# Performance work log

Hardware: AMD Instinct MI355X
Metric: run time of the kernel (lower is better)

The kernel has to match this reference:

```python
import jax, jax.numpy as jnp
import numpy as np

B, S, D_IN, HEAD_DIM = 4, 4096, 1024, 128

def setup_inputs() -> dict:
    key = jax.random.key(0)
    k1, k2, k3, k4 = jax.random.split(key, 4)
    x = jax.random.normal(k1, (B, S, D_IN), dtype=jnp.float32)
    # nn.Parameter(torch.rand(...)) -> uniform [0,1)
    W_query = jax.random.uniform(k2, (D_IN, HEAD_DIM), dtype=jnp.float32)
    W_key = jax.random.uniform(k3, (D_IN, HEAD_DIM), dtype=jnp.float32)
    W_value = jax.random.uniform(k4, (D_IN, HEAD_DIM), dtype=jnp.float32)
    return {"x": x, "W_query": W_query, "W_key": W_key, "W_value": W_value}

def reference(x, W_query, W_key, W_value):
    # x: [B,S,d_in]; W_*: [d_in,head_dim]
    queries = jnp.einsum('bsd,dh->bsh', x, W_query)
    keys = jnp.einsum('bsd,dh->bsh', x, W_key)
    values = jnp.einsum('bsd,dh->bsh', x, W_value)
    scale = 1.0 / jnp.sqrt(jnp.asarray(HEAD_DIM, dtype=x.dtype))
    attn_scores = jnp.einsum('bqh,bkh->bqk', queries, keys)  # [B,S,S]
    attn_weights = jax.nn.softmax(attn_scores * scale, axis=-1)
    context_vec = jnp.einsum('bqk,bkh->bqh', attn_weights, values)
    return context_vec
```

## Files before the change

kernel.cpp:

```cpp
#include <hip/hip_runtime.h>
#include <cstdint>

#define B_  4
#define S_  4096
#define DIN 1024
#define DH  128
#define QSCALE (0.08838834764831845f * 1.4426950408889634f)

typedef short bf16x8 __attribute__((ext_vector_type(8)));
typedef float f32x4 __attribute__((ext_vector_type(4)));
typedef unsigned short u16;
typedef unsigned int   u32;

#define MFMA16(a, b, c) __builtin_amdgcn_mfma_f32_16x16x32_bf16(a, b, c, 0, 0, 0)

#define GLOAD_LDS16(g, l) __builtin_amdgcn_global_load_lds( \
    (const __attribute__((address_space(1))) void*)(g),     \
    (__attribute__((address_space(3))) void*)(l), 16, 0, 0)

#if __has_builtin(__builtin_amdgcn_exp2f)
#define EXP2(x) __builtin_amdgcn_exp2f(x)
#else
#define EXP2(x) exp2f(x)
#endif

__device__ inline u16 bf16_rn(float f) {
    union { float f; u32 u; } v; v.f = f;
    u32 r = v.u + 0x7FFFu + ((v.u >> 16) & 1u);
    return (u16)(r >> 16);
}
__device__ inline float bf16_f(u16 h) {
    union { u32 u; float f; } v; v.u = ((u32)h) << 16; return v.f;
}
__device__ inline u32 pk2(float a, float b) {
    return (u32)bf16_rn(a) | ((u32)bf16_rn(b) << 16);
}
__device__ inline void split2(float a, float b, u32& hi, u32& lo) {
    u32 ua = __builtin_bit_cast(u32, a), ub = __builtin_bit_cast(u32, b);
    u32 ha = ua & 0xFFFF0000u, hb = ub & 0xFFFF0000u;
    hi = (ua >> 16) | hb;
    float la = a - __builtin_bit_cast(float, ha);
    float lb = b - __builtin_bit_cast(float, hb);
    lo = (u32)bf16_rn(la) | ((u32)bf16_rn(lb) << 16);
}

__global__ __launch_bounds__(256) void wconv2(
    const float* __restrict__ Wq, const float* __restrict__ Wk, const float* __restrict__ Wv,
    u16* __restrict__ wpack)
{
    int id  = blockIdx.x * 256 + threadIdx.x;
    int s   = id / 2560;
    int rem = id % 2560;
    int p   = rem >> 9;
    int gi  = rem & 511;
    int n   = gi & 127, kq2 = gi >> 7;
    const float* W = (p < 2) ? Wq : (p < 4) ? Wk : Wv;
    int k0 = 32 * s + 8 * kq2;
    u16 o[8];
    #pragma unroll
    for (int j = 0; j < 8; ++j) {
        float v = W[(size_t)(k0 + j) * DH + n];
        if (p < 2) v *= QSCALE;
        if (p == 4) {
            o[j] = bf16_rn(v);
        } else {
            u32 u = __builtin_bit_cast(u32, v);
            if ((p & 1) == 0) o[j] = (u16)(u >> 16);
            else o[j] = bf16_rn(v - __builtin_bit_cast(float, u & 0xFFFF0000u));
        }
    }
    u16* dst = wpack + (size_t)id * 8;
    *(uint4*)dst = *(uint4*)o;
}

__global__ __launch_bounds__(256) void qkv_v7(
    const float* __restrict__ x, const u16* __restrict__ wpack,
    u16* __restrict__ qhi, u16* __restrict__ qlo,
    u16* __restrict__ khi, u16* __restrict__ klo, u16* __restrict__ vt)
{
    __shared__ __align__(16) char lds[40960];

    const int t    = threadIdx.x;
    const int row0 = blockIdx.x * 64;
    const int lane = t & 63, wave = t >> 6;
    const int l15  = lane & 15, g = lane >> 4;
    const int wr   = wave >> 1, wc = wave & 1;

    f32x4 accq[2][4], acck[2][4], accv[2][4];
    #pragma unroll
    for (int rt = 0; rt < 2; ++rt)
        #pragma unroll
        for (int nt = 0; nt < 4; ++nt)
            #pragma unroll
            for (int r = 0; r < 4; ++r) {
                accq[rt][nt][r] = 0.f; acck[rt][nt][r] = 0.f; accv[rt][nt][r] = 0.f;
            }

    const char* WP = (const char*)wpack;
    auto stage = [&](int s) {
        const char* src = WP + (size_t)s * 40960;
        #pragma unroll
        for (int c = 0; c < 10; ++c) {
            int o = t * 16 + c * 4096;
            GLOAD_LDS16(src + o, lds + o);
        }
    };

    const float* xp0 = x + (size_t)(row0 + 32 * wr + l15) * DIN + 8 * g;
    const float* xp1 = xp0 + (size_t)16 * DIN;

    float4 ca0 = *(const float4*)(xp0);
    float4 cb0 = *(const float4*)(xp0 + 4);
    float4 ca1 = *(const float4*)(xp1);
    float4 cb1 = *(const float4*)(xp1 + 4);

    for (int s = 0; s < 32; ++s) {
        stage(s);

        bf16x8 xh[2], xl[2];
        {
            uint4 H, L;
            split2(ca0.x, ca0.y, H.x, L.x); split2(ca0.z, ca0.w, H.y, L.y);
            split2(cb0.x, cb0.y, H.z, L.z); split2(cb0.z, cb0.w, H.w, L.w);
            xh[0] = __builtin_bit_cast(bf16x8, H);
            xl[0] = __builtin_bit_cast(bf16x8, L);
        }
        {
            uint4 H, L;
            split2(ca1.x, ca1.y, H.x, L.x); split2(ca1.z, ca1.w, H.y, L.y);
            split2(cb1.x, cb1.y, H.z, L.z); split2(cb1.z, cb1.w, H.w, L.w);
            xh[1] = __builtin_bit_cast(bf16x8, H);
            xl[1] = __builtin_bit_cast(bf16x8, L);
        }

        __syncthreads();

        float4 na0, nb0, na1, nb1;
        if (s < 31) {
            na0 = *(const float4*)(xp0 + 32 * (s + 1));
            nb0 = *(const float4*)(xp0 + 32 * (s + 1) + 4);
            na1 = *(const float4*)(xp1 + 32 * (s + 1));
            nb1 = *(const float4*)(xp1 + 32 * (s + 1) + 4);
        }

        #pragma unroll
        for (int nt = 0; nt < 4; ++nt) {
            const int n  = 64 * wc + 16 * nt + l15;
            const int wo = (g << 11) + (n << 4);
            bf16x8 qwh = *(const bf16x8*)(lds + wo);
            bf16x8 qwl = *(const bf16x8*)(lds +  8192 + wo);
            bf16x8 kwh = *(const bf16x8*)(lds + 16384 + wo);
            bf16x8 kwl = *(const bf16x8*)(lds + 24576 + wo);
            bf16x8 vwh = *(const bf16x8*)(lds + 32768 + wo);
            #pragma unroll
            for (int rt = 0; rt < 2; ++rt) {
                accq[rt][nt] = MFMA16(xh[rt], qwh, accq[rt][nt]);
                accq[rt][nt] = MFMA16(xl[rt], qwh, accq[rt][nt]);
                accq[rt][nt] = MFMA16(xh[rt], qwl, accq[rt][nt]);
                acck[rt][nt] = MFMA16(xh[rt], kwh, acck[rt][nt]);
                acck[rt][nt] = MFMA16(xl[rt], kwh, acck[rt][nt]);
                acck[rt][nt] = MFMA16(xh[rt], kwl, acck[rt][nt]);
                accv[rt][nt] = MFMA16(xh[rt], vwh, accv[rt][nt]);
            }
        }
        __syncthreads();
        if (s < 31) { ca0 = na0; cb0 = nb0; ca1 = na1; cb1 = nb1; }
    }

    const int bb = row0 >> 12, kt = (row0 & 4095) >> 6;

    #pragma unroll
    for (int rt = 0; rt < 2; ++rt)
        #pragma unroll
        for (int reg = 0; reg < 4; ++reg) {
            int r = row0 + 32 * wr + 16 * rt + 4 * g + reg;
            #pragma unroll
            for (int nt = 0; nt < 4; ++nt) {
                int c = 64 * wc + 16 * nt + l15;
                float v = accq[rt][nt][reg];
                u32 u = __builtin_bit_cast(u32, v);
                float lo = v - __builtin_bit_cast(float, u & 0xFFFF0000u);
                size_t o = (size_t)r * DH + c;
                qhi[o] = (u16)(u >> 16);
                qlo[o] = bf16_rn(lo);
            }
        }

    u16* lk = (u16*)lds;
    #pragma unroll
    for (int rt = 0; rt < 2; ++rt)
        #pragma unroll
        for (int reg = 0; reg < 4; ++reg) {
            int kr = 32 * wr + 16 * rt + 4 * g + reg;
            #pragma unroll
            for (int nt = 0; nt < 4; ++nt) {
                int c = 64 * wc + 16 * nt + l15;
                int o = kr * 128 + (((c >> 3) ^ (kr & 15)) << 3) + (c & 7);
                float v = acck[rt][nt][reg];
                u32 u = __builtin_bit_cast(u32, v);
                lk[o]        = (u16)(u >> 16);
                lk[8192 + o] = bf16_rn(v - __builtin_bit_cast(float, u & 0xFFFF0000u));
            }
        }
    __syncthreads();
    {
        char* gk = (char*)(khi + (size_t)(bb * 64 + kt) * 8192);
        char* gl = (char*)(klo + (size_t)(bb * 64 + kt) * 8192);
        #pragma unroll
        for (int c2 = 0; c2 < 4; ++c2) {
            int o = t * 16 + c2 * 4096;
            *(uint4*)(gk + o) = *(const uint4*)(lds + o);
            *(uint4*)(gl + o) = *(const uint4*)(lds + 16384 + o);
        }
    }
    __syncthreads();

    #pragma unroll
    for (int rt = 0; rt < 2; ++rt)
        #pragma unroll
        for (int reg = 0; reg < 4; ++reg) {
            int kr = 32 * wr + 16 * rt + 4 * g + reg;
            #pragma unroll
            for (int nt = 0; nt < 4; ++nt) {
                int c = 64 * wc + 16 * nt + l15;
                int o = c * 64 + (((kr >> 3) ^ (c & 7)) << 3) + (kr & 7);
                lk[o] = bf16_rn(accv[rt][nt][reg]);
            }
        }
    __syncthreads();
    {
        char* gv = (char*)(vt + (size_t)(bb * 64 + kt) * 8192);
        #pragma unroll
        for (int c2 = 0; c2 < 4; ++c2) {
            int o = t * 16 + c2 * 4096;
            *(uint4*)(gv + o) = *(const uint4*)(lds + o);
        }
    }
}

__global__ __launch_bounds__(512, 2) void flash_db(
    const u16* __restrict__ qhi, const u16* __restrict__ qlo,
    const u16* __restrict__ khi, const u16* __restrict__ klo,
    const u16* __restrict__ vt,
    u16* __restrict__ opart, float2* __restrict__ ml)
{
    __shared__ __align__(16) char smem[2 * 49152];

    const int tid  = threadIdx.x;
    const int wave = tid >> 6, lane = tid & 63;
    const int l15  = lane & 15, g = lane >> 4;
    const int bid  = blockIdx.x;
    const int pair = bid & 15, qt = bid >> 4;
    const int b = pair >> 2, z = pair & 3;

    const int q0row = b * S_ + qt * 256 + wave * 32;

    bf16x8 qh[2][4], ql[2][4];
    #pragma unroll
    for (int h = 0; h < 2; ++h)
        #pragma unroll
        for (int ks = 0; ks < 4; ++ks) {
            size_t qa = (size_t)(q0row + 16 * h + l15) * DH + 32 * ks + 8 * g;
            qh[h][ks] = *(const bf16x8*)(qhi + qa);
            ql[h][ks] = *(const bf16x8*)(qlo + qa);
        }

    f32x4 O0[8], O1[8];
    #pragma unroll
    for (int dt = 0; dt < 8; ++dt)
        #pragma unroll
        for (int r = 0; r < 4; ++r) { O0[dt][r] = 0.f; O1[dt][r] = 0.f; }

    float m0 = -3.0e38f, l0 = 0.f, m1 = -3.0e38f, l1 = 0.f;

    int koff[4];
    #pragma unroll
    for (int ks = 0; ks < 4; ++ks)
        koff[ks] = (((4 * ks + g) ^ l15) << 4) + (l15 << 8);
    int voff[2];
    #pragma unroll
    for (int kw = 0; kw < 2; ++kw)
        voff[kw] = (((4 * kw + g) ^ (l15 & 7)) << 4);

    const char* kbase = (const char*)(khi + (size_t)b * 64 * 8192);
    const char* lbase = (const char*)(klo + (size_t)b * 64 * 8192);
    const char* vbase = (const char*)(vt  + (size_t)b * 64 * 8192);
    const int kt0 = z * 16;

    auto stage = [&](int bufi, int ktl) {
        const char* sk = kbase + (size_t)(kt0 + ktl) * 16384;
        const char* sl = lbase + (size_t)(kt0 + ktl) * 16384;
        const char* sv = vbase + (size_t)(kt0 + ktl) * 16384;
        char* dk = smem + bufi * 49152;
        #pragma unroll
        for (int c = 0; c < 2; ++c) {
            int o = tid * 16 + c * 8192;
            GLOAD_LDS16(sk + o, dk + o);
            GLOAD_LDS16(sl + o, dk + 16384 + o);
            GLOAD_LDS16(sv + o, dk + 32768 + o);
        }
    };

    stage(0, 0);
    __syncthreads();

    int buf = 0;
    for (int ktl = 0; ktl < 16; ++ktl) {
        if (ktl < 15) stage(buf ^ 1, ktl + 1);

        const char* bk = smem + buf * 49152;
        const char* bl = bk + 16384;
        const char* bv = bk + 32768;

        f32x4 s0[4], s1[4];
        #pragma unroll
        for (int nt = 0; nt < 4; ++nt)
            #pragma unroll
            for (int r = 0; r < 4; ++r) { s0[nt][r] = 0.f; s1[nt][r] = 0.f; }

        #pragma unroll
        for (int ks = 0; ks < 4; ++ks) {
            #pragma unroll
            for (int nt = 0; nt < 4; ++nt) {
                bf16x8 kh = *(const bf16x8*)(bk + nt * 4096 + koff[ks]);
                bf16x8 kl = *(const bf16x8*)(bl + nt * 4096 + koff[ks]);
                s0[nt] = MFMA16(kh, qh[0][ks], s0[nt]);
                s0[nt] = MFMA16(kh, ql[0][ks], s0[nt]);
                s0[nt] = MFMA16(kl, qh[0][ks], s0[nt]);
                s1[nt] = MFMA16(kh, qh[1][ks], s1[nt]);
                s1[nt] = MFMA16(kh, ql[1][ks], s1[nt]);
                s1[nt] = MFMA16(kl, qh[1][ks], s1[nt]);
            }
        }

        float ml0 = -3.0e38f, ml1 = -3.0e38f;
        #pragma unroll
        for (int nt = 0; nt < 4; ++nt)
            #pragma unroll
            for (int r = 0; r < 4; ++r) {
                ml0 = fmaxf(ml0, s0[nt][r]);
                ml1 = fmaxf(ml1, s1[nt][r]);
            }
        ml0 = fmaxf(ml0, __shfl_xor(ml0, 16));
        ml0 = fmaxf(ml0, __shfl_xor(ml0, 32));
        ml1 = fmaxf(ml1, __shfl_xor(ml1, 16));
        ml1 = fmaxf(ml1, __shfl_xor(ml1, 32));

        if (!__all((ml0 <= m0 + 8.0f) & (ml1 <= m1 + 8.0f))) {
            float mn0 = fmaxf(m0, ml0), mn1 = fmaxf(m1, ml1);
            float fsc0 = EXP2(m0 - mn0), fsc1 = EXP2(m1 - mn1);
            m0 = mn0; m1 = mn1;
            l0 *= fsc0; l1 *= fsc1;
            float fr0[4], fr1[4];
            #pragma unroll
            for (int r = 0; r < 4; ++r) {
                fr0[r] = __shfl(fsc0, 4 * g + r);
                fr1[r] = __shfl(fsc1, 4 * g + r);
            }
            #pragma unroll
            for (int dt = 0; dt < 8; ++dt)
                #pragma unroll
                for (int r = 0; r < 4; ++r) {
                    O0[dt][r] *= fr0[r];
                    O1[dt][r] *= fr1[r];
                }
        }

        u32 pk0[4][2], pk1[4][2];
        float ps0 = 0.f, ps1 = 0.f;
        #pragma unroll
        for (int nt = 0; nt < 4; ++nt) {
            float a0 = EXP2(s0[nt][0] - m0), a1 = EXP2(s0[nt][1] - m0);
            float a2 = EXP2(s0[nt][2] - m0), a3 = EXP2(s0[nt][3] - m0);
            ps0 += (a0 + a1) + (a2 + a3);
            pk0[nt][0] = pk2(a0, a1);
            pk0[nt][1] = pk2(a2, a3);
            float c0 = EXP2(s1[nt][0] - m1), c1 = EXP2(s1[nt][1] - m1);
            float c2 = EXP2(s1[nt][2] - m1), c3 = EXP2(s1[nt][3] - m1);
            ps1 += (c0 + c1) + (c2 + c3);
            pk1[nt][0] = pk2(c0, c1);
            pk1[nt][1] = pk2(c2, c3);
        }
        ps0 += __shfl_xor(ps0, 16);
        ps0 += __shfl_xor(ps0, 32);
        ps1 += __shfl_xor(ps1, 16);
        ps1 += __shfl_xor(ps1, 32);
        l0 += ps0; l1 += ps1;

        const int s0l = l15 | ((2 * (g & 1)) << 4);
        const int s1l = s0l + 16;
        const int hiH = g >> 1;
        #pragma unroll
        for (int kw = 0; kw < 2; ++kw) {
            u32 a0, a1, a2, a3, c0, c1, c2, c3;
            {
                u32 x0 = __shfl(pk0[2 * kw][0], s0l), y0 = __shfl(pk0[2 * kw + 1][0], s0l);
                u32 x1 = __shfl(pk0[2 * kw][1], s0l), y1 = __shfl(pk0[2 * kw + 1][1], s0l);
                u32 x2 = __shfl(pk0[2 * kw][0], s1l), y2 = __shfl(pk0[2 * kw + 1][0], s1l);
                u32 x3 = __shfl(pk0[2 * kw][1], s1l), y3 = __shfl(pk0[2 * kw + 1][1], s1l);
                a0 = hiH ? y0 : x0; a1 = hiH ? y1 : x1;
                a2 = hiH ? y2 : x2; a3 = hiH ? y3 : x3;
            }
            {
                u32 x0 = __shfl(pk1[2 * kw][0], s0l), y0 = __shfl(pk1[2 * kw + 1][0], s0l);
                u32 x1 = __shfl(pk1[2 * kw][1], s0l), y1 = __shfl(pk1[2 * kw + 1][1], s0l);
                u32 x2 = __shfl(pk1[2 * kw][0], s1l), y2 = __shfl(pk1[2 * kw + 1][0], s1l);
                u32 x3 = __shfl(pk1[2 * kw][1], s1l), y3 = __shfl(pk1[2 * kw + 1][1], s1l);
                c0 = hiH ? y0 : x0; c1 = hiH ? y1 : x1;
                c2 = hiH ? y2 : x2; c3 = hiH ? y3 : x3;
            }
            union { u32 w[4]; bf16x8 v; } pa, pb;
            pa.w[0] = a0; pa.w[1] = a1; pa.w[2] = a2; pa.w[3] = a3;
            pb.w[0] = c0; pb.w[1] = c1; pb.w[2] = c2; pb.w[3] = c3;
            #pragma unroll
            for (int dt = 0; dt < 8; ++dt) {
                bf16x8 vf = *(const bf16x8*)(bv + (16 * dt + l15) * 128 + voff[kw]);
                O0[dt] = MFMA16(pa.v, vf, O0[dt]);
                O1[dt] = MFMA16(pb.v, vf, O1[dt]);
            }
        }

        __syncthreads();
        buf ^= 1;
    }

    u16* op = opart + ((size_t)z * 16384 + q0row) * DH;
    #pragma unroll
    for (int dt = 0; dt < 8; ++dt)
        #pragma unroll
        for (int r = 0; r < 4; ++r) {
            op[(size_t)(4 * g + r) * DH + 16 * dt + l15]      = bf16_rn(O0[dt][r]);
            op[(size_t)(16 + 4 * g + r) * DH + 16 * dt + l15] = bf16_rn(O1[dt][r]);
        }
    if (lane < 16) {
        ml[(size_t)z * 16384 + q0row + lane]      = make_float2(m0, l0);
        ml[(size_t)z * 16384 + q0row + 16 + lane] = make_float2(m1, l1);
    }
}

__global__ __launch_bounds__(256) void merge4(
    const u16* __restrict__ op, const float2* __restrict__ ml, float* __restrict__ O)
{
    int row = blockIdx.x * 16 + (threadIdx.x >> 4);
    int dq  = (threadIdx.x & 15) * 8;
    float2 a[4];
    #pragma unroll
    for (int zz = 0; zz < 4; ++zz) a[zz] = ml[(size_t)zz * 16384 + row];
    float M = fmaxf(fmaxf(a[0].x, a[1].x), fmaxf(a[2].x, a[3].x));
    float w[4], den = 0.f;
    #pragma unroll
    for (int zz = 0; zz < 4; ++zz) {
        w[zz] = EXP2(a[zz].x - M);
        den += a[zz].y * w[zz];
    }
    float inv = 1.0f / den;
    float acc[8];
    #pragma unroll
    for (int j = 0; j < 8; ++j) acc[j] = 0.f;
    #pragma unroll
    for (int zz = 0; zz < 4; ++zz) {
        const u16* p = op + ((size_t)zz * 16384 + row) * DH + dq;
        bf16x8 vv = *(const bf16x8*)p;
        #pragma unroll
        for (int j = 0; j < 8; ++j) acc[j] += w[zz] * bf16_f((u16)vv[j]);
    }
    float4 oa, ob;
    oa.x = acc[0] * inv; oa.y = acc[1] * inv; oa.z = acc[2] * inv; oa.w = acc[3] * inv;
    ob.x = acc[4] * inv; ob.y = acc[5] * inv; ob.z = acc[6] * inv; ob.w = acc[7] * inv;
    *(float4*)(O + (size_t)row * DH + dq)     = oa;
    *(float4*)(O + (size_t)row * DH + dq + 4) = ob;
}

extern "C" void kernel_launch(void* const* d_in, const int* in_sizes, int n_in,
                              void* d_out, int out_size, void* d_ws, size_t ws_size,
                              hipStream_t stream) {
    const float* x  = (const float*)d_in[0];
    const float* Wq = (const float*)d_in[1];
    const float* Wk = (const float*)d_in[2];
    const float* Wv = (const float*)d_in[3];
    float* out = (float*)d_out;

    const size_t SZ = (size_t)B_ * S_ * DH;
    u16* qhi = (u16*)d_ws;
    u16* qlo = qhi + SZ;
    u16* khi = qlo + SZ;
    u16* klo = khi + SZ;
    u16* vtp = klo + SZ;
    u16* wpk = vtp + SZ;
    u16* opart = wpk + 655360;
    float2* mlp = (float2*)((char*)opart + (size_t)4 * 16384 * DH * 2);

    wconv2<<<320, 256, 0, stream>>>(Wq, Wk, Wv, wpk);
    qkv_v7<<<256, 256, 0, stream>>>(x, wpk, qhi, qlo, khi, klo, vtp);
    flash_db<<<256, 512, 0, stream>>>(qhi, qlo, khi, klo, vtp, opart, mlp);
    merge4<<<1024, 256, 0, stream>>>(opart, mlp, out);
}
```

Measured before the change: 144.2 us.

## Double-buffer weight staging and use 8 waves per block in QKV projection

The QKV projection kernel now runs 512 threads (8 waves), each wave handling 16 rows instead of 32. Weight slices are double-buffered in 80KB of LDS, so the async global-to-LDS copy of the next k-slice overlaps the MFMAs on the current one, and one barrier per iteration is removed. This aims to hide weight-load latency and raise wave-level parallelism. In exchange it halves per-wave reuse of each weight LDS read and the larger LDS footprint limits blocks per CU.

```diff
diff --git a/kernel.cpp b/kernel.cpp
--- a/kernel.cpp
+++ b/kernel.cpp
@@ -73,142 +73,127 @@
     *(uint4*)dst = *(uint4*)o;
 }
 
-__global__ __launch_bounds__(256) void qkv_v7(
+__global__ __launch_bounds__(512) void qkv_v8(
     const float* __restrict__ x, const u16* __restrict__ wpack,
     u16* __restrict__ qhi, u16* __restrict__ qlo,
     u16* __restrict__ khi, u16* __restrict__ klo, u16* __restrict__ vt)
 {
-    __shared__ __align__(16) char lds[40960];
+    __shared__ __align__(16) char lds[81920];
 
     const int t    = threadIdx.x;
     const int row0 = blockIdx.x * 64;
     const int lane = t & 63, wave = t >> 6;
     const int l15  = lane & 15, g = lane >> 4;
-    const int wr   = wave >> 1, wc = wave & 1;
-
-    f32x4 accq[2][4], acck[2][4], accv[2][4];
-    #pragma unroll
-    for (int rt = 0; rt < 2; ++rt)
-        #pragma unroll
-        for (int nt = 0; nt < 4; ++nt)
-            #pragma unroll
-            for (int r = 0; r < 4; ++r) {
-                accq[rt][nt][r] = 0.f; acck[rt][nt][r] = 0.f; accv[rt][nt][r] = 0.f;
-            }
+    const int wr   = wave >> 1;
+    const int wc   = wave & 1;
+
+    f32x4 accq[4], acck[4], accv[4];
+    #pragma unroll
+    for (int nt = 0; nt < 4; ++nt)
+        #pragma unroll
+        for (int r = 0; r < 4; ++r) {
+            accq[nt][r] = 0.f; acck[nt][r] = 0.f; accv[nt][r] = 0.f;
+        }
 
     const char* WP = (const char*)wpack;
-    auto stage = [&](int s) {
+    auto stage = [&](int bufi, int s) {
+        char* d = lds + bufi * 40960;
         const char* src = WP + (size_t)s * 40960;
         #pragma unroll
-        for (int c = 0; c < 10; ++c) {
-            int o = t * 16 + c * 4096;
-            GLOAD_LDS16(src + o, lds + o);
+        for (int c = 0; c < 5; ++c) {
+            int o = t * 16 + c * 8192;
+            GLOAD_LDS16(src + o, d + o);
         }
     };
 
-    const float* xp0 = x + (size_t)(row0 + 32 * wr + l15) * DIN + 8 * g;
-    const float* xp1 = xp0 + (size_t)16 * DIN;
-
-    float4 ca0 = *(const float4*)(xp0);
-    float4 cb0 = *(const float4*)(xp0 + 4);
-    float4 ca1 = *(const float4*)(xp1);
-    float4 cb1 = *(const float4*)(xp1 + 4);
-
+    const float* xp = x + (size_t)(row0 + 16 * wr + l15) * DIN + 8 * g;
+
+    float4 ca = *(const float4*)(xp);
+    float4 cb = *(const float4*)(xp + 4);
+
+    stage(0, 0);
+    __syncthreads();
+
+    int buf = 0;
     for (int s = 0; s < 32; ++s) {
-        stage(s);
-
-        bf16x8 xh[2], xl[2];
+        if (s < 31) stage(buf ^ 1, s + 1);
+
+        float4 na, nb;
+        if (s < 31) {
+            na = *(const float4*)(xp + 32 * (s + 1));
+            nb = *(const float4*)(xp + 32 * (s + 1) + 4);
+        }
+
+        bf16x8 xh, xl;
         {
             uint4 H, L;
-            split2(ca0.x, ca0.y, H.x, L.x); split2(ca0.z, ca0.w, H.y, L.y);
-            split2(cb0.x, cb0.y, H.z, L.z); split2(cb0.z, cb0.w, H.w, L.w);
-            xh[0] = __builtin_bit_cast(bf16x8, H);
-            xl[0] = __builtin_bit_cast(bf16x8, L);
-        }
-        {
-            uint4 H, L;
-            split2(ca1.x, ca1.y, H.x, L.x); split2(ca1.z, ca1.w, H.y, L.y);
-            split2(cb1.x, cb1.y, H.z, L.z); split2(cb1.z, cb1.w, H.w, L.w);
-            xh[1] = __builtin_bit_cast(bf16x8, H);
-            xl[1] = __builtin_bit_cast(bf16x8, L);
-        }
-
-        __syncthreads();
-
-        float4 na0, nb0, na1, nb1;
-        if (s < 31) {
-            na0 = *(const float4*)(xp0 + 32 * (s + 1));
-            nb0 = *(const float4*)(xp0 + 32 * (s + 1) + 4);
-            na1 = *(const float4*)(xp1 + 32 * (s + 1));
-            nb1 = *(const float4*)(xp1 + 32 * (s + 1) + 4);
-        }
-
+            split2(ca.x, ca.y, H.x, L.x); split2(ca.z, ca.w, H.y, L.y);
+            split2(cb.x, cb.y, H.z, L.z); split2(cb.z, cb.w, H.w, L.w);
+            xh = __builtin_bit_cast(bf16x8, H);
+            xl = __builtin_bit_cast(bf16x8, L);
+        }
+
+        const char* wb = lds + buf * 40960;
         #pragma unroll
         for (int nt = 0; nt < 4; ++nt) {
             const int n  = 64 * wc + 16 * nt + l15;
             const int wo = (g << 11) + (n << 4);
-            bf16x8 qwh = *(const bf16x8*)(lds + wo);
-            bf16x8 qwl = *(const bf16x8*)(lds +  8192 + wo);
-            bf16x8 kwh = *(const bf16x8*)(lds + 16384 + wo);
-            bf16x8 kwl = *(const bf16x8*)(lds + 24576 + wo);
-            bf16x8 vwh = *(const bf16x8*)(lds + 32768 + wo);
-            #pragma unroll
-            for (int rt = 0; rt < 2; ++rt) {
-                accq[rt][nt] = MFMA16(xh[rt], qwh, accq[rt][nt]);
-                accq[rt][nt] = MFMA16(xl[rt], qwh, accq[rt][nt]);
-                accq[rt][nt] = MFMA16(xh[rt], qwl, accq[rt][nt]);
-                acck[rt][nt] = MFMA16(xh[rt], kwh, acck[rt][nt]);
-                acck[rt][nt] = MFMA16(xl[rt], kwh, acck[rt][nt]);
-                acck[rt][nt] = MFMA16(xh[rt], kwl, acck[rt][nt]);
-                accv[rt][nt] = MFMA16(xh[rt], vwh, accv[rt][nt]);
-            }
+            bf16x8 qwh = *(const bf16x8*)(wb + wo);
+            bf16x8 qwl = *(const bf16x8*)(wb +  8192 + wo);
+            bf16x8 kwh = *(const bf16x8*)(wb + 16384 + wo);
+            bf16x8 kwl = *(const bf16x8*)(wb + 24576 + wo);
+            bf16x8 vwh = *(const bf16x8*)(wb + 32768 + wo);
+            accq[nt] = MFMA16(xh, qwh, accq[nt]);
+            accq[nt] = MFMA16(xl, qwh, accq[nt]);
+            accq[nt] = MFMA16(xh, qwl, accq[nt]);
+            acck[nt] = MFMA16(xh, kwh, acck[nt]);
+            acck[nt] = MFMA16(xl, kwh, acck[nt]);
+            acck[nt] = MFMA16(xh, kwl, acck[nt]);
+            accv[nt] = MFMA16(xh, vwh, accv[nt]);
         }
         __syncthreads();
-        if (s < 31) { ca0 = na0; cb0 = nb0; ca1 = na1; cb1 = nb1; }
+        if (s < 31) { ca = na; cb = nb; }
+        buf ^= 1;
     }
 
     const int bb = row0 >> 12, kt = (row0 & 4095) >> 6;
 
     #pragma unroll
-    for (int rt = 0; rt < 2; ++rt)
-        #pragma unroll
-        for (int reg = 0; reg < 4; ++reg) {
-            int r = row0 + 32 * wr + 16 * rt + 4 * g + reg;
-            #pragma unroll
-            for (int nt = 0; nt < 4; ++nt) {
-                int c = 64 * wc + 16 * nt + l15;
-                float v = accq[rt][nt][reg];
-                u32 u = __builtin_bit_cast(u32, v);
-                float lo = v - __builtin_bit_cast(float, u & 0xFFFF0000u);
-                size_t o = (size_t)r * DH + c;
-                qhi[o] = (u16)(u >> 16);
-                qlo[o] = bf16_rn(lo);
-            }
-        }
+    for (int reg = 0; reg < 4; ++reg) {
+        int r = row0 + 16 * wr + 4 * g + reg;
+        #pragma unroll
+        for (int nt = 0; nt < 4; ++nt) {
+            int c = 64 * wc + 16 * nt + l15;
+            float v = accq[nt][reg];
+            u32 u = __builtin_bit_cast(u32, v);
+            float lo = v - __builtin_bit_cast(float, u & 0xFFFF0000u);
+            size_t o = (size_t)r * DH + c;
+            qhi[o] = (u16)(u >> 16);
+            qlo[o] = bf16_rn(lo);
+        }
+    }
 
     u16* lk = (u16*)lds;
     #pragma unroll
-    for (int rt = 0; rt < 2; ++rt)
-        #pragma unroll
-        for (int reg = 0; reg < 4; ++reg) {
-            int kr = 32 * wr + 16 * rt + 4 * g + reg;
-            #pragma unroll
-            for (int nt = 0; nt < 4; ++nt) {
-                int c = 64 * wc + 16 * nt + l15;
-                int o = kr * 128 + (((c >> 3) ^ (kr & 15)) << 3) + (c & 7);
-                float v = acck[rt][nt][reg];
-                u32 u = __builtin_bit_cast(u32, v);
-                lk[o]        = (u16)(u >> 16);
-                lk[8192 + o] = bf16_rn(v - __builtin_bit_cast(float, u & 0xFFFF0000u));
-            }
-        }
+    for (int reg = 0; reg < 4; ++reg) {
+        int kr = 16 * wr + 4 * g + reg;
+        #pragma unroll
+        for (int nt = 0; nt < 4; ++nt) {
+            int c = 64 * wc + 16 * nt + l15;
+            int o = kr * 128 + (((c >> 3) ^ (kr & 15)) << 3) + (c & 7);
+            float v = acck[nt][reg];
+            u32 u = __builtin_bit_cast(u32, v);
+            lk[o]        = (u16)(u >> 16);
+            lk[8192 + o] = bf16_rn(v - __builtin_bit_cast(float, u & 0xFFFF0000u));
+        }
+    }
     __syncthreads();
     {
         char* gk = (char*)(khi + (size_t)(bb * 64 + kt) * 8192);
         char* gl = (char*)(klo + (size_t)(bb * 64 + kt) * 8192);
         #pragma unroll
-        for (int c2 = 0; c2 < 4; ++c2) {
-            int o = t * 16 + c2 * 4096;
+        for (int c2 = 0; c2 < 2; ++c2) {
+            int o = t * 16 + c2 * 8192;
             *(uint4*)(gk + o) = *(const uint4*)(lds + o);
             *(uint4*)(gl + o) = *(const uint4*)(lds + 16384 + o);
         }
@@ -216,23 +201,21 @@
     __syncthreads();
 
     #pragma unroll
-    for (int rt = 0; rt < 2; ++rt)
-        #pragma unroll
-        for (int reg = 0; reg < 4; ++reg) {
-            int kr = 32 * wr + 16 * rt + 4 * g + reg;
-            #pragma unroll
-            for (int nt = 0; nt < 4; ++nt) {
-                int c = 64 * wc + 16 * nt + l15;
-                int o = c * 64 + (((kr >> 3) ^ (c & 7)) << 3) + (kr & 7);
-                lk[o] = bf16_rn(accv[rt][nt][reg]);
-            }
-        }
+    for (int reg = 0; reg < 4; ++reg) {
+        int kr = 16 * wr + 4 * g + reg;
+        #pragma unroll
+        for (int nt = 0; nt < 4; ++nt) {
+            int c = 64 * wc + 16 * nt + l15;
+            int o = c * 64 + (((kr >> 3) ^ (c & 7)) << 3) + (kr & 7);
+            lk[o] = bf16_rn(accv[nt][reg]);
+        }
+    }
     __syncthreads();
     {
         char* gv = (char*)(vt + (size_t)(bb * 64 + kt) * 8192);
         #pragma unroll
-        for (int c2 = 0; c2 < 4; ++c2) {
-            int o = t * 16 + c2 * 4096;
+        for (int c2 = 0; c2 < 2; ++c2) {
+            int o = t * 16 + c2 * 8192;
             *(uint4*)(gv + o) = *(const uint4*)(lds + o);
         }
     }
@@ -491,7 +474,7 @@
     float2* mlp = (float2*)((char*)opart + (size_t)4 * 16384 * DH * 2);
 
     wconv2<<<320, 256, 0, stream>>>(Wq, Wk, Wv, wpk);
-    qkv_v7<<<256, 256, 0, stream>>>(x, wpk, qhi, qlo, khi, klo, vtp);
+    qkv_v8<<<256, 512, 0, stream>>>(x, wpk, qhi, qlo, khi, klo, vtp);
     flash_db<<<256, 512, 0, stream>>>(qhi, qlo, khi, klo, vtp, opart, mlp);
     merge4<<<1024, 256, 0, stream>>>(opart, mlp, out);
 }
```

Result: faster. 127.9 us (-11.4%).
